# Optimization experiments

Hardware: AMD Instinct MI355X
Metric: run time of the kernel (lower is better)

Reference implementation:

```python
import jax, jax.numpy as jnp
import numpy as np
import math

QUERY_DIM = 1024
KEY_DIM = 768
VALUE_DIM = 768
NUM_HEADS = 16
HEAD_DIM = QUERY_DIM // NUM_HEADS


def setup_inputs() -> dict:
    key = jax.random.key(0)
    ks = jax.random.split(key, 11)
    B, Sq, Skv = 4, 2048, 2048
    query = jax.random.normal(ks[0], (B, Sq, QUERY_DIM), dtype=jnp.float32)
    k_in = jax.random.normal(ks[1], (B, Skv, KEY_DIM), dtype=jnp.float32)
    v_in = jax.random.normal(ks[2], (B, Skv, VALUE_DIM), dtype=jnp.float32)
    # Linear weights stored as [in, out] (y = x @ W + b), equivalent to torch's x @ W^T.
    def lin(k, fan_in, fan_out):
        bound = 1.0 / math.sqrt(fan_in)
        kw, kb = jax.random.split(k)
        W = jax.random.uniform(kw, (fan_in, fan_out), minval=-bound, maxval=bound, dtype=jnp.float32)
        b = jax.random.uniform(kb, (fan_out,), minval=-bound, maxval=bound, dtype=jnp.float32)
        return W, b
    Wq, bq = lin(ks[3], QUERY_DIM, QUERY_DIM)
    Wk, bk = lin(ks[4], KEY_DIM, QUERY_DIM)
    Wv, bv = lin(ks[5], VALUE_DIM, QUERY_DIM)
    Wo, bo = lin(ks[6], QUERY_DIM, QUERY_DIM)
    return {"query": query, "key": k_in, "value": v_in,
            "Wq": Wq, "bq": bq, "Wk": Wk, "bk": bk,
            "Wv": Wv, "bv": bv, "Wo": Wo, "bo": bo}


def reference(query, key, value, Wq, bq, Wk, bk, Wv, bv, Wo, bo):
    B, Sq, _ = query.shape
    H, D = NUM_HEADS, HEAD_DIM
    # Projections -> [B, H, S, D]
    Q = (query @ Wq + bq).reshape(B, Sq, H, D).transpose(0, 2, 1, 3)
    K = (key @ Wk + bk).reshape(B, -1, H, D).transpose(0, 2, 1, 3)
    V = (value @ Wv + bv).reshape(B, -1, H, D).transpose(0, 2, 1, 3)
    scale = 1.0 / math.sqrt(D)
    scores = jnp.einsum('bhqd,bhkd->bhqk', Q, K) * scale  # [B,H,Sq,Skv]
    weights = jax.nn.softmax(scores, axis=-1)
    attended = jnp.einsum('bhqk,bhkd->bhqd', weights, V)
    attended = attended.transpose(0, 2, 1, 3).reshape(B, Sq, H * D)
    # torch .squeeze(1): no-op since Sq > 1
    return attended @ Wo + bo
```

## Files before the change

kernel.cpp:

```cpp
#include <hip/hip_runtime.h>

#define B_ 4
#define SQ 2048
#define SKV 2048
#define DMODEL 1024
#define DKV 768
#define NH 16
#define DH 64

typedef unsigned short u16;
typedef __bf16 bf16x4 __attribute__((ext_vector_type(4)));
typedef __bf16 bf16x8 __attribute__((ext_vector_type(8)));
typedef float f32x4 __attribute__((ext_vector_type(4)));
typedef float f32x16 __attribute__((ext_vector_type(16)));

__device__ __forceinline__ u16 f2bf(float f) {
  union { __bf16 b; u16 u; } cv;
  cv.b = (__bf16)f;
  return cv.u;
}

__device__ __forceinline__ unsigned cvtpk(float lo, float hi) {
  unsigned r;
  asm("v_cvt_pk_bf16_f32 %0, %1, %2" : "=v"(r) : "v"(lo), "v"(hi));
  return r;
}

__device__ __forceinline__ float fexp2(float x) {
  float r;
  asm("v_exp_f32 %0, %1" : "=v"(r) : "v"(x));
  return r;
}

#define GLDS(gp, lp) __builtin_amdgcn_global_load_lds(                         \
    (const __attribute__((address_space(1))) unsigned*)(gp),                   \
    (__attribute__((address_space(3))) unsigned*)(lp), 16, 0, 0)

__global__ __launch_bounds__(256)
void wt4_kernel(const float* __restrict__ W0, const float* __restrict__ W1,
                const float* __restrict__ W2, const float* __restrict__ W3,
                u16* __restrict__ T0, u16* __restrict__ T1,
                u16* __restrict__ T2, u16* __restrict__ T3) {
  const int z = blockIdx.z;
  const float* W = (z == 0) ? W0 : (z == 1) ? W1 : (z == 2) ? W2 : W3;
  u16* T = (z == 0) ? T0 : (z == 1) ? T1 : (z == 2) ? T2 : T3;
  const int K = (z == 1 || z == 2) ? DKV : DMODEL;
  const int N = DMODEL;
  int n0 = blockIdx.x * 32, k0 = blockIdx.y * 32;
  if (k0 >= K) return;
  __shared__ float tl[32][33];
  int tx = threadIdx.x, ty = threadIdx.y;
#pragma unroll
  for (int p = 0; p < 4; ++p)
    tl[ty + 8 * p][tx] = W[(size_t)(k0 + ty + 8 * p) * N + n0 + tx];
  __syncthreads();
#pragma unroll
  for (int p = 0; p < 4; ++p)
    T[(size_t)(n0 + ty + 8 * p) * K + k0 + tx] = f2bf(tl[tx][ty + 8 * p]);
}

template<int A_IS_BF16, int OUT_MODE>
__global__ __launch_bounds__(256)
void gemm_kernel(const void* __restrict__ A_, const u16* __restrict__ Wt,
                 const float* __restrict__ bias, float oscale, void* __restrict__ out_,
                 int M, int N, int K) {
  constexpr int AP = A_IS_BF16 ? 64 : 88;
  __shared__ __align__(16) u16 Alds[128][AP];
  __shared__ __align__(16) u16 Blds[128][64];
  const int t = threadIdx.x;
  const int l = t & 63;
  const int lx = l & 15, lg = l >> 4;
  const int wid = t >> 6;
  const int wr = wid >> 1, wc = wid & 1;

  int bx, by;
  if (gridDim.x == 8 && (gridDim.y & 7) == 0) {
    int flat = blockIdx.y * 8 + blockIdx.x;
    by = (flat & 7) * 8 + ((flat >> 3) & 7);
    bx = flat >> 6;
  } else { bx = blockIdx.x; by = blockIdx.y; }
  const int m0 = by * 128, n0 = bx * 128;

  const int srow = l >> 3;
  const int scol = (l & 7) * 8;

  f32x4 acc[4][4];
#pragma unroll
  for (int i = 0; i < 4; ++i)
#pragma unroll
    for (int j = 0; j < 4; ++j) acc[i][j] = (f32x4){0.f, 0.f, 0.f, 0.f};

  const float* Af = (const float*)A_;
  const u16* Ab = (const u16*)A_;
  const int arow = t >> 4;
  const int acol = (t & 15) * 4;
  const float* abase = Af + (size_t)(m0 + arow) * K + acol;

  float4 areg[8];
  if (!A_IS_BF16) {
#pragma unroll
    for (int p = 0; p < 8; ++p)
      areg[p] = *(const float4*)(abase + (size_t)p * 16 * K);
  }

  for (int k0 = 0; k0 < K; k0 += 64) {
    __syncthreads();
#pragma unroll
    for (int j = 0; j < 4; ++j) {
      int row = wid * 32 + j * 8;
      GLDS(Wt + (size_t)(n0 + row + srow) * K + k0 + scol, &Blds[row][0]);
    }
    if (A_IS_BF16) {
#pragma unroll
      for (int j = 0; j < 4; ++j) {
        int row = wid * 32 + j * 8;
        GLDS(Ab + (size_t)(m0 + row + srow) * K + k0 + scol, &Alds[row][0]);
      }
    } else {
#pragma unroll
      for (int p = 0; p < 8; ++p) {
        union { bf16x4 v; uint2 u; } cv;
        cv.v[0] = (__bf16)areg[p].x; cv.v[1] = (__bf16)areg[p].y;
        cv.v[2] = (__bf16)areg[p].z; cv.v[3] = (__bf16)areg[p].w;
        *(uint2*)(&Alds[p * 16 + arow][acol]) = cv.u;
      }
    }
    __syncthreads();
    if (!A_IS_BF16 && (k0 + 64) < K) {
#pragma unroll
      for (int p = 0; p < 8; ++p)
        areg[p] = *(const float4*)(abase + (size_t)p * 16 * K + k0 + 64);
    }
#pragma unroll
    for (int kk = 0; kk < 64; kk += 32) {
      bf16x8 af[4], bfr[4];
#pragma unroll
      for (int i = 0; i < 4; ++i)
        af[i] = *(const bf16x8*)(&Alds[wr * 64 + i * 16 + lx][kk + lg * 8]);
#pragma unroll
      for (int j = 0; j < 4; ++j)
        bfr[j] = *(const bf16x8*)(&Blds[wc * 64 + j * 16 + lx][kk + lg * 8]);
#pragma unroll
      for (int i = 0; i < 4; ++i)
#pragma unroll
        for (int j = 0; j < 4; ++j)
          acc[i][j] = __builtin_amdgcn_mfma_f32_16x16x32_bf16(af[i], bfr[j], acc[i][j], 0, 0, 0);
    }
  }
#pragma unroll
  for (int j = 0; j < 4; ++j) {
    int col = n0 + wc * 64 + j * 16 + lx;
    float bv = bias[col];
#pragma unroll
    for (int i = 0; i < 4; ++i) {
      int rowb = m0 + wr * 64 + i * 16 + lg * 4;
      f32x4 c = acc[i][j];
      if (OUT_MODE == 2) {
        int b = rowb >> 11, s = rowb & 2047;
        int h = col >> 6, d = col & 63;
        u16* vt = (u16*)out_ + (size_t)((b * NH + h) * DH + d) * SKV + s;
        unsigned w0 = cvtpk((c[0] + bv) * oscale, (c[1] + bv) * oscale);
        unsigned w1 = cvtpk((c[2] + bv) * oscale, (c[3] + bv) * oscale);
        *(uint2*)vt = make_uint2(w0, w1);
      } else {
#pragma unroll
        for (int r = 0; r < 4; ++r) {
          float val = (c[r] + bv) * oscale;
          if (OUT_MODE == 1) ((float*)out_)[(size_t)(rowb + r) * N + col] = val;
          else               ((u16*)out_)[(size_t)(rowb + r) * N + col] = f2bf(val);
        }
      }
    }
  }
}

#define KVB 64
#define KP 72

__global__ __launch_bounds__(256)
void attn_kernel(const u16* __restrict__ Qp, const u16* __restrict__ Kp,
                 const u16* __restrict__ Vt, u16* __restrict__ Att) {
  __shared__ __align__(16) u16 Klds[2][KVB][KP];
  __shared__ __align__(16) u16 Vlds[2][DH][KP];
  const int t = threadIdx.x;
  const int l = t & 63;
  const int ql = l & 31, hi = l >> 5;
  const int wid = t >> 6;

  const int flat = blockIdx.y * 16 + blockIdx.x;
  const int xcd = flat & 7;
  const int rest = flat >> 3;
  const int bh = xcd * 8 + (rest & 7);
  const int qb = rest >> 3;
  const int b = bh >> 4, h = bh & 15;
  const int q = qb * 128 + wid * 32 + ql;

  bf16x8 qf[4];
  const u16* qbase = Qp + (size_t)(b * SQ + q) * DMODEL + h * 64 + hi * 8;
#pragma unroll
  for (int ds = 0; ds < 4; ++ds) qf[ds] = *(const bf16x8*)(qbase + ds * 16);

  bf16x8 ones;
  {
    union { unsigned u[4]; bf16x8 v; } o;
    o.u[0] = o.u[1] = o.u[2] = o.u[3] = 0x3F803F80u;
    ones = o.v;
  }
  f32x16 z16;
#pragma unroll
  for (int r = 0; r < 16; ++r) z16[r] = 0.f;

  f32x16 acc0, acc1, sacc;
#pragma unroll
  for (int r = 0; r < 16; ++r) { acc0[r] = 0.f; acc1[r] = 0.f; sacc[r] = 0.f; }

  const int sr = t >> 2;
  const int sc = (t & 3) * 16;
  const u16* kg = Kp + (size_t)(b * SKV) * DMODEL + h * 64;
  const u16* vg = Vt + ((size_t)(b * NH + h) * DH + sr) * SKV;

  {
    const u16* kp_ = kg + (size_t)sr * DMODEL + sc;
    uint4 k0 = *(const uint4*)kp_, k1 = *(const uint4*)(kp_ + 8);
    uint4 v0 = *(const uint4*)(vg + sc), v1 = *(const uint4*)(vg + sc + 8);
    *(uint4*)(&Klds[0][sr][sc]) = k0; *(uint4*)(&Klds[0][sr][sc + 8]) = k1;
    *(uint4*)(&Vlds[0][sr][sc]) = v0; *(uint4*)(&Vlds[0][sr][sc + 8]) = v1;
  }
  int cur = 0;

  for (int kv0 = 0; kv0 < SKV; kv0 += KVB) {
    uint4 kr0, kr1, vr0, vr1;
    const bool pf = (kv0 + KVB) < SKV;
    if (pf) {
      const u16* kp_ = kg + (size_t)(kv0 + KVB + sr) * DMODEL + sc;
      kr0 = *(const uint4*)kp_; kr1 = *(const uint4*)(kp_ + 8);
      const u16* vp_ = vg + kv0 + KVB + sc;
      vr0 = *(const uint4*)vp_; vr1 = *(const uint4*)(vp_ + 8);
    }
    __syncthreads();

    f32x16 st0, st1;
    __builtin_amdgcn_s_setprio(1);
    {
      bf16x8 k0 = *(const bf16x8*)(&Klds[cur][ql][hi * 8]);
      bf16x8 k1 = *(const bf16x8*)(&Klds[cur][32 + ql][hi * 8]);
      st0 = __builtin_amdgcn_mfma_f32_32x32x16_bf16(k0, qf[0], z16, 0, 0, 0);
      st1 = __builtin_amdgcn_mfma_f32_32x32x16_bf16(k1, qf[0], z16, 0, 0, 0);
    }
#pragma unroll
    for (int ds = 1; ds < 4; ++ds) {
      bf16x8 k0 = *(const bf16x8*)(&Klds[cur][ql][ds * 16 + hi * 8]);
      bf16x8 k1 = *(const bf16x8*)(&Klds[cur][32 + ql][ds * 16 + hi * 8]);
      st0 = __builtin_amdgcn_mfma_f32_32x32x16_bf16(k0, qf[ds], st0, 0, 0, 0);
      st1 = __builtin_amdgcn_mfma_f32_32x32x16_bf16(k1, qf[ds], st1, 0, 0, 0);
    }
    __builtin_amdgcn_s_setprio(0);

#pragma unroll
    for (int r = 0; r < 16; ++r) { st0[r] = fexp2(st0[r]); st1[r] = fexp2(st1[r]); }

    __builtin_amdgcn_s_setprio(1);
#pragma unroll
    for (int tt = 0; tt < 2; ++tt) {
      const f32x16& stt = tt ? st1 : st0;
      unsigned pk[8];
#pragma unroll
      for (int j = 0; j < 8; ++j) pk[j] = cvtpk(stt[2 * j], stt[2 * j + 1]);
#pragma unroll
      for (int ksl = 0; ksl < 2; ++ksl) {
        auto wA = __builtin_amdgcn_permlane32_swap(pk[4 * ksl + 0], pk[4 * ksl + 2], false, false);
        auto wB = __builtin_amdgcn_permlane32_swap(pk[4 * ksl + 1], pk[4 * ksl + 3], false, false);
        union { unsigned w[4]; bf16x8 v; } pfr;
        pfr.w[0] = (unsigned)wA[0]; pfr.w[1] = (unsigned)wB[0];
        pfr.w[2] = (unsigned)wA[1]; pfr.w[3] = (unsigned)wB[1];
        int ks = tt * 2 + ksl;
        bf16x8 v0 = *(const bf16x8*)(&Vlds[cur][ql][ks * 16 + hi * 8]);
        bf16x8 v1 = *(const bf16x8*)(&Vlds[cur][32 + ql][ks * 16 + hi * 8]);
        acc0 = __builtin_amdgcn_mfma_f32_32x32x16_bf16(v0, pfr.v, acc0, 0, 0, 0);
        acc1 = __builtin_amdgcn_mfma_f32_32x32x16_bf16(v1, pfr.v, acc1, 0, 0, 0);
        sacc = __builtin_amdgcn_mfma_f32_32x32x16_bf16(ones, pfr.v, sacc, 0, 0, 0);
      }
    }
    __builtin_amdgcn_s_setprio(0);

    if (pf) {
      int nxt = cur ^ 1;
      *(uint4*)(&Klds[nxt][sr][sc]) = kr0; *(uint4*)(&Klds[nxt][sr][sc + 8]) = kr1;
      *(uint4*)(&Vlds[nxt][sr][sc]) = vr0; *(uint4*)(&Vlds[nxt][sr][sc + 8]) = vr1;
    }
    cur ^= 1;
  }

  float inv = 1.0f / sacc[0];
  u16* ob = Att + (size_t)(b * SQ + q) * DMODEL + h * 64;
#pragma unroll
  for (int dt = 0; dt < 2; ++dt) {
    const f32x16& a = dt ? acc1 : acc0;
#pragma unroll
    for (int g = 0; g < 4; ++g) {
      unsigned w0 = cvtpk(a[4 * g] * inv, a[4 * g + 1] * inv);
      unsigned w1 = cvtpk(a[4 * g + 2] * inv, a[4 * g + 3] * inv);
      *(uint2*)(ob + dt * 32 + g * 8 + hi * 4) = make_uint2(w0, w1);
    }
  }
}

extern "C" void kernel_launch(void* const* d_in, const int* in_sizes, int n_in,
                              void* d_out, int out_size, void* d_ws, size_t ws_size,
                              hipStream_t stream) {
  const float* query = (const float*)d_in[0];
  const float* key   = (const float*)d_in[1];
  const float* value = (const float*)d_in[2];
  const float* Wq = (const float*)d_in[3];
  const float* bq = (const float*)d_in[4];
  const float* Wk = (const float*)d_in[5];
  const float* bk = (const float*)d_in[6];
  const float* Wv = (const float*)d_in[7];
  const float* bv = (const float*)d_in[8];
  const float* Wo = (const float*)d_in[9];
  const float* bo = (const float*)d_in[10];
  float* out = (float*)d_out;

  u16* ws = (u16*)d_ws;
  const size_t MTOK = (size_t)B_ * SQ;
  u16* Qp  = ws;
  u16* Kp  = Qp + MTOK * DMODEL;
  u16* Vtb = Kp + MTOK * DMODEL;
  u16* Att = Vtb + MTOK * DMODEL;
  u16* WqT = Att + MTOK * DMODEL;
  u16* WkT = WqT + (size_t)DMODEL * DMODEL;
  u16* WvT = WkT + (size_t)DKV * DMODEL;
  u16* WoT = WvT + (size_t)DKV * DMODEL;

  const float SCL = 0.18033688011112042f;

  dim3 tb(32, 8);
  wt4_kernel<<<dim3(DMODEL / 32, DMODEL / 32, 4), tb, 0, stream>>>(
      Wq, Wk, Wv, Wo, WqT, WkT, WvT, WoT);

  gemm_kernel<0, 0><<<dim3(DMODEL / 128, MTOK / 128), 256, 0, stream>>>(query, WqT, bq, SCL, Qp, (int)MTOK, DMODEL, DMODEL);
  gemm_kernel<0, 0><<<dim3(DMODEL / 128, MTOK / 128), 256, 0, stream>>>(key,   WkT, bk, 1.0f, Kp, (int)MTOK, DMODEL, DKV);
  gemm_kernel<0, 2><<<dim3(DMODEL / 128, MTOK / 128), 256, 0, stream>>>(value, WvT, bv, 1.0f, Vtb, (int)MTOK, DMODEL, DKV);

  attn_kernel<<<dim3(SQ / 128, B_ * NH), 256, 0, stream>>>(Qp, Kp, Vtb, Att);

  gemm_kernel<1, 1><<<dim3(DMODEL / 128, MTOK / 128), 256, 0, stream>>>(Att, WoT, bo, 1.0f, out, (int)MTOK, DMODEL, DMODEL);
}
```

Baseline: 208.8 us.

## Batch QKV projections into one launch and interleave attention K halves per wave

The three separate Q/K/V projection GEMM launches become a single launch with a z-dimension selecting the operand set. This lets all 1536 blocks run concurrently and removes launch gaps and tail effects. Inside the attention loop, each wave now processes the two 32-row K halves sequentially (score, exp, PV) instead of computing both score tiles first. Waves with different parity start on different halves, which cuts live registers and spreads LDS bank access. The O-projection becomes a dedicated bf16-input kernel with the same logic.

New measurement: 204.0 us. 1.02x faster.

```diff
diff --git a/kernel.cpp b/kernel.cpp
--- a/kernel.cpp
+++ b/kernel.cpp
@@ -59,13 +59,120 @@
     T[(size_t)(n0 + ty + 8 * p) * K + k0 + tx] = f2bf(tl[tx][ty + 8 * p]);
 }
 
-template<int A_IS_BF16, int OUT_MODE>
 __global__ __launch_bounds__(256)
-void gemm_kernel(const void* __restrict__ A_, const u16* __restrict__ Wt,
-                 const float* __restrict__ bias, float oscale, void* __restrict__ out_,
-                 int M, int N, int K) {
-  constexpr int AP = A_IS_BF16 ? 64 : 88;
-  __shared__ __align__(16) u16 Alds[128][AP];
+void qkv_kernel(const float* __restrict__ Aq, const float* __restrict__ Ak,
+                const float* __restrict__ Av,
+                const u16* __restrict__ Wtq, const u16* __restrict__ Wtk,
+                const u16* __restrict__ Wtv,
+                const float* __restrict__ bq, const float* __restrict__ bk,
+                const float* __restrict__ bv,
+                float sclq,
+                u16* __restrict__ Qp, u16* __restrict__ Kp, u16* __restrict__ Vt) {
+  __shared__ __align__(16) u16 Alds[128][88];
+  __shared__ __align__(16) u16 Blds[128][64];
+  const int z = blockIdx.z;
+  const float* Af = (z == 0) ? Aq : (z == 1) ? Ak : Av;
+  const u16* Wt = (z == 0) ? Wtq : (z == 1) ? Wtk : Wtv;
+  const float* bias = (z == 0) ? bq : (z == 1) ? bk : bv;
+  const int K = (z == 0) ? DMODEL : DKV;
+  const float oscale = (z == 0) ? sclq : 1.0f;
+
+  const int t = threadIdx.x;
+  const int l = t & 63;
+  const int lx = l & 15, lg = l >> 4;
+  const int wid = t >> 6;
+  const int wr = wid >> 1, wc = wid & 1;
+
+  int flat = blockIdx.y * 8 + blockIdx.x;
+  int by = (flat & 7) * 8 + ((flat >> 3) & 7);
+  int bx = flat >> 6;
+  const int m0 = by * 128, n0 = bx * 128;
+
+  const int srow = l >> 3;
+  const int scol = (l & 7) * 8;
+
+  f32x4 acc[4][4];
+#pragma unroll
+  for (int i = 0; i < 4; ++i)
+#pragma unroll
+    for (int j = 0; j < 4; ++j) acc[i][j] = (f32x4){0.f, 0.f, 0.f, 0.f};
+
+  const int arow = t >> 4;
+  const int acol = (t & 15) * 4;
+  const float* abase = Af + (size_t)(m0 + arow) * K + acol;
+
+  float4 areg[8];
+#pragma unroll
+  for (int p = 0; p < 8; ++p)
+    areg[p] = *(const float4*)(abase + (size_t)p * 16 * K);
+
+  for (int k0 = 0; k0 < K; k0 += 64) {
+    __syncthreads();
+#pragma unroll
+    for (int j = 0; j < 4; ++j) {
+      int row = wid * 32 + j * 8;
+      GLDS(Wt + (size_t)(n0 + row + srow) * K + k0 + scol, &Blds[row][0]);
+    }
+#pragma unroll
+    for (int p = 0; p < 8; ++p) {
+      union { bf16x4 v; uint2 u; } cv;
+      cv.v[0] = (__bf16)areg[p].x; cv.v[1] = (__bf16)areg[p].y;
+      cv.v[2] = (__bf16)areg[p].z; cv.v[3] = (__bf16)areg[p].w;
+      *(uint2*)(&Alds[p * 16 + arow][acol]) = cv.u;
+    }
+    __syncthreads();
+    if ((k0 + 64) < K) {
+#pragma unroll
+      for (int p = 0; p < 8; ++p)
+        areg[p] = *(const float4*)(abase + (size_t)p * 16 * K + k0 + 64);
+    }
+#pragma unroll
+    for (int kk = 0; kk < 64; kk += 32) {
+      bf16x8 af[4], bfr[4];
+#pragma unroll
+      for (int i = 0; i < 4; ++i)
+        af[i] = *(const bf16x8*)(&Alds[wr * 64 + i * 16 + lx][kk + lg * 8]);
+#pragma unroll
+      for (int j = 0; j < 4; ++j)
+        bfr[j] = *(const bf16x8*)(&Blds[wc * 64 + j * 16 + lx][kk + lg * 8]);
+#pragma unroll
+      for (int i = 0; i < 4; ++i)
+#pragma unroll
+        for (int j = 0; j < 4; ++j)
+          acc[i][j] = __builtin_amdgcn_mfma_f32_16x16x32_bf16(af[i], bfr[j], acc[i][j], 0, 0, 0);
+    }
+  }
+#pragma unroll
+  for (int j = 0; j < 4; ++j) {
+    int col = n0 + wc * 64 + j * 16 + lx;
+    float bv = bias[col];
+#pragma unroll
+    for (int i = 0; i < 4; ++i) {
+      int rowb = m0 + wr * 64 + i * 16 + lg * 4;
+      f32x4 c = acc[i][j];
+      if (z == 2) {
+        int b = rowb >> 11, s = rowb & 2047;
+        int h = col >> 6, d = col & 63;
+        u16* vt = Vt + (size_t)((b * NH + h) * DH + d) * SKV + s;
+        union { bf16x4 v; uint2 u; } cv;
+        cv.v[0] = (__bf16)(c[0] + bv); cv.v[1] = (__bf16)(c[1] + bv);
+        cv.v[2] = (__bf16)(c[2] + bv); cv.v[3] = (__bf16)(c[3] + bv);
+        *(uint2*)vt = cv.u;
+      } else {
+        u16* op = (z == 0) ? Qp : Kp;
+#pragma unroll
+        for (int r = 0; r < 4; ++r)
+          op[(size_t)(rowb + r) * DMODEL + col] = f2bf((c[r] + bv) * oscale);
+      }
+    }
+  }
+}
+
+__global__ __launch_bounds__(256)
+void oproj_kernel(const u16* __restrict__ Ab, const u16* __restrict__ Wt,
+                  const float* __restrict__ bias, float* __restrict__ out_) {
+  const int M = B_ * SQ, N = DMODEL, K = DMODEL;
+  __shared__ __align__(16) u16 Alds[128][64];
   __shared__ __align__(16) u16 Blds[128][64];
   const int t = threadIdx.x;
   const int l = t & 63;
@@ -73,12 +180,9 @@
   const int wid = t >> 6;
   const int wr = wid >> 1, wc = wid & 1;
 
-  int bx, by;
-  if (gridDim.x == 8 && (gridDim.y & 7) == 0) {
-    int flat = blockIdx.y * 8 + blockIdx.x;
-    by = (flat & 7) * 8 + ((flat >> 3) & 7);
-    bx = flat >> 6;
-  } else { bx = blockIdx.x; by = blockIdx.y; }
+  int flat = blockIdx.y * 8 + blockIdx.x;
+  int by = (flat & 7) * 8 + ((flat >> 3) & 7);
+  int bx = flat >> 6;
   const int m0 = by * 128, n0 = bx * 128;
 
   const int srow = l >> 3;
@@ -89,19 +193,6 @@
   for (int i = 0; i < 4; ++i)
 #pragma unroll
     for (int j = 0; j < 4; ++j) acc[i][j] = (f32x4){0.f, 0.f, 0.f, 0.f};
-
-  const float* Af = (const float*)A_;
-  const u16* Ab = (const u16*)A_;
-  const int arow = t >> 4;
-  const int acol = (t & 15) * 4;
-  const float* abase = Af + (size_t)(m0 + arow) * K + acol;
-
-  float4 areg[8];
-  if (!A_IS_BF16) {
-#pragma unroll
-    for (int p = 0; p < 8; ++p)
-      areg[p] = *(const float4*)(abase + (size_t)p * 16 * K);
-  }
 
   for (int k0 = 0; k0 < K; k0 += 64) {
     __syncthreads();
@@ -109,28 +200,9 @@
     for (int j = 0; j < 4; ++j) {
       int row = wid * 32 + j * 8;
       GLDS(Wt + (size_t)(n0 + row + srow) * K + k0 + scol, &Blds[row][0]);
-    }
-    if (A_IS_BF16) {
-#pragma unroll
-      for (int j = 0; j < 4; ++j) {
-        int row = wid * 32 + j * 8;
-        GLDS(Ab + (size_t)(m0 + row + srow) * K + k0 + scol, &Alds[row][0]);
-      }
-    } else {
-#pragma unroll
-      for (int p = 0; p < 8; ++p) {
-        union { bf16x4 v; uint2 u; } cv;
-        cv.v[0] = (__bf16)areg[p].x; cv.v[1] = (__bf16)areg[p].y;
-        cv.v[2] = (__bf16)areg[p].z; cv.v[3] = (__bf16)areg[p].w;
-        *(uint2*)(&Alds[p * 16 + arow][acol]) = cv.u;
-      }
+      GLDS(Ab + (size_t)(m0 + row + srow) * K + k0 + scol, &Alds[row][0]);
     }
     __syncthreads();
-    if (!A_IS_BF16 && (k0 + 64) < K) {
-#pragma unroll
-      for (int p = 0; p < 8; ++p)
-        areg[p] = *(const float4*)(abase + (size_t)p * 16 * K + k0 + 64);
-    }
 #pragma unroll
     for (int kk = 0; kk < 64; kk += 32) {
       bf16x8 af[4], bfr[4];
@@ -155,21 +227,9 @@
     for (int i = 0; i < 4; ++i) {
       int rowb = m0 + wr * 64 + i * 16 + lg * 4;
       f32x4 c = acc[i][j];
-      if (OUT_MODE == 2) {
-        int b = rowb >> 11, s = rowb & 2047;
-        int h = col >> 6, d = col & 63;
-        u16* vt = (u16*)out_ + (size_t)((b * NH + h) * DH + d) * SKV + s;
-        unsigned w0 = cvtpk((c[0] + bv) * oscale, (c[1] + bv) * oscale);
-        unsigned w1 = cvtpk((c[2] + bv) * oscale, (c[3] + bv) * oscale);
-        *(uint2*)vt = make_uint2(w0, w1);
-      } else {
-#pragma unroll
-        for (int r = 0; r < 4; ++r) {
-          float val = (c[r] + bv) * oscale;
-          if (OUT_MODE == 1) ((float*)out_)[(size_t)(rowb + r) * N + col] = val;
-          else               ((u16*)out_)[(size_t)(rowb + r) * N + col] = f2bf(val);
-        }
-      }
+#pragma unroll
+      for (int r = 0; r < 4; ++r)
+        out_[(size_t)(rowb + r) * N + col] = c[r] + bv;
     }
   }
 }
@@ -227,6 +287,7 @@
     *(uint4*)(&Vlds[0][sr][sc]) = v0; *(uint4*)(&Vlds[0][sr][sc + 8]) = v1;
   }
   int cur = 0;
+  const int h0 = wid & 1;
 
   for (int kv0 = 0; kv0 < SKV; kv0 += KVB) {
     uint4 kr0, kr1, vr0, vr1;
@@ -239,33 +300,31 @@
     }
     __syncthreads();
 
-    f32x16 st0, st1;
-    __builtin_amdgcn_s_setprio(1);
-    {
-      bf16x8 k0 = *(const bf16x8*)(&Klds[cur][ql][hi * 8]);
-      bf16x8 k1 = *(const bf16x8*)(&Klds[cur][32 + ql][hi * 8]);
-      st0 = __builtin_amdgcn_mfma_f32_32x32x16_bf16(k0, qf[0], z16, 0, 0, 0);
-      st1 = __builtin_amdgcn_mfma_f32_32x32x16_bf16(k1, qf[0], z16, 0, 0, 0);
-    }
-#pragma unroll
-    for (int ds = 1; ds < 4; ++ds) {
-      bf16x8 k0 = *(const bf16x8*)(&Klds[cur][ql][ds * 16 + hi * 8]);
-      bf16x8 k1 = *(const bf16x8*)(&Klds[cur][32 + ql][ds * 16 + hi * 8]);
-      st0 = __builtin_amdgcn_mfma_f32_32x32x16_bf16(k0, qf[ds], st0, 0, 0, 0);
-      st1 = __builtin_amdgcn_mfma_f32_32x32x16_bf16(k1, qf[ds], st1, 0, 0, 0);
-    }
-    __builtin_amdgcn_s_setprio(0);
-
-#pragma unroll
-    for (int r = 0; r < 16; ++r) { st0[r] = fexp2(st0[r]); st1[r] = fexp2(st1[r]); }
-
-    __builtin_amdgcn_s_setprio(1);
-#pragma unroll
-    for (int tt = 0; tt < 2; ++tt) {
-      const f32x16& stt = tt ? st1 : st0;
+#pragma unroll
+    for (int ph = 0; ph < 2; ++ph) {
+      const int hf = ph ^ h0;
+      const int krow = hf * 32 + ql;
+      f32x16 st;
+      __builtin_amdgcn_s_setprio(1);
+      {
+        bf16x8 k0 = *(const bf16x8*)(&Klds[cur][krow][hi * 8]);
+        st = __builtin_amdgcn_mfma_f32_32x32x16_bf16(k0, qf[0], z16, 0, 0, 0);
+      }
+#pragma unroll
+      for (int ds = 1; ds < 4; ++ds) {
+        bf16x8 kk = *(const bf16x8*)(&Klds[cur][krow][ds * 16 + hi * 8]);
+        st = __builtin_amdgcn_mfma_f32_32x32x16_bf16(kk, qf[ds], st, 0, 0, 0);
+      }
+      __builtin_amdgcn_s_setprio(0);
+
+#pragma unroll
+      for (int r = 0; r < 16; ++r) st[r] = fexp2(st[r]);
+
       unsigned pk[8];
 #pragma unroll
-      for (int j = 0; j < 8; ++j) pk[j] = cvtpk(stt[2 * j], stt[2 * j + 1]);
+      for (int j = 0; j < 8; ++j) pk[j] = cvtpk(st[2 * j], st[2 * j + 1]);
+
+      __builtin_amdgcn_s_setprio(1);
 #pragma unroll
       for (int ksl = 0; ksl < 2; ++ksl) {
         auto wA = __builtin_amdgcn_permlane32_swap(pk[4 * ksl + 0], pk[4 * ksl + 2], false, false);
@@ -273,15 +332,15 @@
         union { unsigned w[4]; bf16x8 v; } pfr;
         pfr.w[0] = (unsigned)wA[0]; pfr.w[1] = (unsigned)wB[0];
         pfr.w[2] = (unsigned)wA[1]; pfr.w[3] = (unsigned)wB[1];
-        int ks = tt * 2 + ksl;
+        int ks = hf * 2 + ksl;
         bf16x8 v0 = *(const bf16x8*)(&Vlds[cur][ql][ks * 16 + hi * 8]);
         bf16x8 v1 = *(const bf16x8*)(&Vlds[cur][32 + ql][ks * 16 + hi * 8]);
         acc0 = __builtin_amdgcn_mfma_f32_32x32x16_bf16(v0, pfr.v, acc0, 0, 0, 0);
         acc1 = __builtin_amdgcn_mfma_f32_32x32x16_bf16(v1, pfr.v, acc1, 0, 0, 0);
         sacc = __builtin_amdgcn_mfma_f32_32x32x16_bf16(ones, pfr.v, sacc, 0, 0, 0);
       }
-    }
-    __builtin_amdgcn_s_setprio(0);
+      __builtin_amdgcn_s_setprio(0);
+    }
 
     if (pf) {
       int nxt = cur ^ 1;
@@ -338,11 +397,10 @@
   wt4_kernel<<<dim3(DMODEL / 32, DMODEL / 32, 4), tb, 0, stream>>>(
       Wq, Wk, Wv, Wo, WqT, WkT, WvT, WoT);
 
-  gemm_kernel<0, 0><<<dim3(DMODEL / 128, MTOK / 128), 256, 0, stream>>>(query, WqT, bq, SCL, Qp, (int)MTOK, DMODEL, DMODEL);
-  gemm_kernel<0, 0><<<dim3(DMODEL / 128, MTOK / 128), 256, 0, stream>>>(key,   WkT, bk, 1.0f, Kp, (int)MTOK, DMODEL, DKV);
-  gemm_kernel<0, 2><<<dim3(DMODEL / 128, MTOK / 128), 256, 0, stream>>>(value, WvT, bv, 1.0f, Vtb, (int)MTOK, DMODEL, DKV);
+  qkv_kernel<<<dim3(DMODEL / 128, MTOK / 128, 3), 256, 0, stream>>>(
+      query, key, value, WqT, WkT, WvT, bq, bk, bv, SCL, Qp, Kp, Vtb);
 
   attn_kernel<<<dim3(SQ / 128, B_ * NH), 256, 0, stream>>>(Qp, Kp, Vtb, Att);
 
-  gemm_kernel<1, 1><<<dim3(DMODEL / 128, MTOK / 128), 256, 0, stream>>>(Att, WoT, bo, 1.0f, out, (int)MTOK, DMODEL, DMODEL);
-}
+  oproj_kernel<<<dim3(DMODEL / 128, MTOK / 128), 256, 0, stream>>>(Att, WoT, bo, out);
+}
```
